# Optimization experiments

Hardware: AMD Instinct MI355X
Metric: run time of the kernel (lower is better)

Reference implementation:

```python
import jax, jax.numpy as jnp
import numpy as np

A = 20000        # distinct library arcs
T = 500000       # timing arcs in design
S = 8            # LUT slew-axis length
C = 8            # LUT load-axis length
G = 250000       # gates
TOTAL_U = 1000000  # gate x candidate-master entries
SCALE = 1.0e15
MAX_CAP = 1.0e-12
MAX_ITER = 3


def _axis_interval(ax, x):
    """ax: [M,K] monotone axes, x: [M]. Returns lower index i0 in [0,K-2] and frac a (may extrapolate)."""
    K = ax.shape[1]
    i0 = jnp.clip(jnp.sum(ax <= x[:, None], axis=1) - 1, 0, K - 2)
    ar = jnp.arange(ax.shape[0])
    x0 = ax[ar, i0]
    x1 = ax[ar, i0 + 1]
    a = (x - x0) / (x1 - x0)
    return i0, a


def _bilinear_gate(in_slew, load, dtab, stab, axs, axc):
    """Batched bilinear interpolation into per-arc 2D LUTs. All leading dims M."""
    M = in_slew.shape[0]
    ar = jnp.arange(M)
    i0, a = _axis_interval(axs, in_slew)
    j0, b = _axis_interval(axc, load)
    i1, j1 = i0 + 1, j0 + 1

    def _blerp(t):
        return ((1 - a) * (1 - b) * t[ar, i0, j0]
                + (1 - a) * b * t[ar, i0, j1]
                + a * (1 - b) * t[ar, i1, j0]
                + a * b * t[ar, i1, j1])

    return _blerp(dtab), _blerp(stab)


def _compute_ceff_batch(in_slew, c1, c2, rpi, dtab, stab, axs, axc, max_iter=MAX_ITER):
    ceff = jnp.maximum(c1 + c2, 1e-30)
    for _ in range(max_iter):
        d, _ = _bilinear_gate(in_slew, ceff, dtab, stab, axs, axc)
        tau = jnp.maximum(d, 1e-30)
        ratio = jnp.minimum(2.0 * tau / jnp.maximum(in_slew, 1e-30), 10.0)
        h = jnp.where(ratio > 0.01, (1.0 - jnp.exp(-ratio)) / ratio, 1.0 - ratio / 2.0)
        ceff = jnp.maximum(c1 + c2 * h, 1e-30)
    return ceff


def _segment_softmax(logits, gate_id, num_groups):
    """Numerically stable per-gate softmax via segment reductions."""
    gmax = jax.ops.segment_max(logits, gate_id, num_segments=num_groups)
    ex = jnp.exp(logits - gmax[gate_id])
    gsum = jax.ops.segment_sum(ex, gate_id, num_segments=num_groups)
    return ex / gsum[gate_id]


def _gate_grouped_forward(in_arr, in_slew, c1, c2, rpi, arc_idx_r, arc_idx_f,
                          unateness, delay_table, slew_table, load_index, slew_index):
    t = arc_idx_r.shape[0]
    arc_flat = jnp.stack([arc_idx_r, arc_idx_f], axis=1).reshape(-1)  # [2T]
    una = unateness[arc_flat]
    is_fall = jnp.arange(2 * t, dtype=una.dtype) % 2
    rf_idx = (una ^ is_fall).reshape(t, 2)  # rise/fall select per column
    in_slew_sel = jnp.take_along_axis(in_slew, rf_idx, axis=1).reshape(-1)
    in_arr_sel = jnp.take_along_axis(in_arr, rf_idx, axis=1).reshape(-1)

    dtab = delay_table[arc_flat]   # [2T,S,C] big gather (memory bound)
    stab = slew_table[arc_flat]
    axc = load_index[arc_flat]     # [2T,C]
    axs = slew_index[arc_flat]     # [2T,S]

    c1_f = jnp.repeat(c1, 2) / SCALE
    c2_f = jnp.repeat(c2, 2) / SCALE
    rpi_f = jnp.repeat(rpi, 2)
    load = _compute_ceff_batch(in_slew_sel, c1_f, c2_f, rpi_f, dtab, stab, axs, axc)
    load = jnp.minimum(load, MAX_CAP)

    arc_delay, arc_slew = _bilinear_gate(in_slew_sel, load, dtab, stab, axs, axc)
    arr_out = (in_arr_sel + arc_delay).reshape(t, 2)
    slew_out = arc_slew.reshape(t, 2)
    return jnp.concatenate([arr_out, slew_out], axis=1)  # [T,4]


def setup_inputs() -> dict:
    key = jax.random.key(0)
    ks = jax.random.split(key, 14)
    U_flat = jax.random.normal(ks[0], (TOTAL_U,), jnp.float32)
    gate_id = jnp.sort(jax.random.randint(ks[1], (TOTAL_U,), 0, G, dtype=jnp.int32))
    in_arr = jax.random.normal(ks[2], (T, 2), jnp.float32)
    in_slew = jax.random.uniform(ks[3], (T, 2), jnp.float32, 0.05, 3.0)
    c1 = jax.random.uniform(ks[4], (T,), jnp.float32, 0.0, 1.0)
    c2 = jax.random.uniform(ks[5], (T,), jnp.float32, 0.0, 1.0)
    rpi = jax.random.uniform(ks[6], (T,), jnp.float32, 0.1, 1.0)
    arc_idx_r = jax.random.randint(ks[7], (T,), 0, A, dtype=jnp.int32)
    arc_idx_f = jax.random.randint(ks[8], (T,), 0, A, dtype=jnp.int32)
    unateness = jax.random.randint(ks[9], (A,), 0, 2, dtype=jnp.int32)
    delay_table = jax.random.uniform(ks[10], (A, S, C), jnp.float32, 0.01, 1.0)
    slew_table = jax.random.uniform(ks[11], (A, S, C), jnp.float32, 0.01, 1.0)
    # strictly increasing LUT axes: slew axis ~[0.05, 4], load axis ~[5e-17, 3e-15]
    slew_index = jnp.cumsum(jax.random.uniform(ks[12], (A, S), jnp.float32, 0.05, 0.6), axis=1)
    load_index = jnp.cumsum(jax.random.uniform(ks[13], (A, C), jnp.float32, 0.05, 0.6), axis=1) * 1e-15
    return dict(U_flat=U_flat, gate_id=gate_id, in_arr=in_arr, in_slew=in_slew,
                c1=c1, c2=c2, rpi=rpi, arc_idx_r=arc_idx_r, arc_idx_f=arc_idx_f,
                unateness=unateness, delay_table=delay_table, slew_table=slew_table,
                slew_index=slew_index, load_index=load_index)


def reference(U_flat, gate_id, in_arr, in_slew, c1, c2, rpi, arc_idx_r, arc_idx_f,
              unateness, delay_table, slew_table, slew_index, load_index):
    weights = _segment_softmax(U_flat, gate_id, G)  # per-gate soft master selection
    out = _gate_grouped_forward(in_arr, in_slew, c1, c2, rpi, arc_idx_r, arc_idx_f,
                                unateness, delay_table, slew_table, load_index, slew_index)
    return out, weights
```

## Files before the change

### kernel.cpp

```cpp
#include <hip/hip_runtime.h>

#define T_N 500000
#define U_N 1000000
#define G_N 250000
#define A_N 20000

#define SBLK 256
#define HALO 96

#define TIMING_BLOCKS ((T_N + 255) / 256)
#define SOFTMAX_BLOCKS ((U_N + SBLK - 1) / SBLK)

__device__ __forceinline__ float sel8(const float (&r)[8], int j) {
    float v = r[0];
#pragma unroll
    for (int k = 1; k < 8; ++k) v = (j >= k) ? r[k] : v;
    return v;
}

__device__ __forceinline__ void load8(const float* __restrict__ p, float (&r)[8]) {
    const float4* q = (const float4*)p;
    float4 a = q[0], b = q[1];
    r[0]=a.x; r[1]=a.y; r[2]=a.z; r[3]=a.w;
    r[4]=b.x; r[5]=b.y; r[6]=b.z; r[7]=b.w;
}


__global__ void __launch_bounds__(256)
fused_kernel(
             const float2* __restrict__ in_arr,
             const float2* __restrict__ in_slew,
             const float* __restrict__ c1,
             const float* __restrict__ c2,
             const int* __restrict__ arc_r,
             const int* __restrict__ arc_f,
             const int* __restrict__ una,
             const float* __restrict__ dtab,
             const float* __restrict__ stab,
             const float* __restrict__ sidx,
             const float* __restrict__ lidx,
             float4* __restrict__ out,
             const float* __restrict__ U,
             const int* __restrict__ gid,
             float* __restrict__ wout)
{
    __shared__ float se[SBLK + 2 * HALO];
    __shared__ int   sg[SBLK + 2 * HALO];

    if (blockIdx.x >= TIMING_BLOCKS) {
        int sblk = blockIdx.x - TIMING_BLOCKS;
        int base = sblk * SBLK;
        int wstart = base - HALO;

        for (int k = threadIdx.x; k < SBLK + 2 * HALO; k += SBLK) {
            int idx = wstart + k;
            if (idx >= 0 && idx < U_N) {
                se[k] = expf(U[idx]);
                sg[k] = gid[idx];
            } else {
                se[k] = 0.0f;
                sg[k] = -1 - k;
            }
        }
        __syncthreads();

        int i = base + threadIdx.x;
        if (i >= U_N) return;

        int li = threadIdx.x + HALO;
        int g = sg[li];
        float mye = se[li];
        float s = mye;
        for (int j = li - 1; j >= 0 && sg[j] == g; --j) s += se[j];
        for (int j = li + 1; j < SBLK + 2 * HALO && sg[j] == g; ++j) s += se[j];

        wout[i] = mye / s;
        return;
    }

    int t = blockIdx.x * blockDim.x + threadIdx.x;
    if (t >= T_N) return;

    float2 ia = in_arr[t];
    float2 is = in_slew[t];
    float c1f = c1[t] / 1.0e15f;
    float c2f = c2[t] / 1.0e15f;
    int arcs0 = arc_r[t];
    int arcs1 = arc_f[t];

    float res_arr[2], res_slew[2];

#pragma unroll
    for (int col = 0; col < 2; ++col) {
        int arc = (col == 0) ? arcs0 : arcs1;
        int u   = una[arc];
        int rf  = u ^ col;
        float slew = rf ? is.y : is.x;
        float arr  = rf ? ia.y : ia.x;

        float s[8], cx[8];
        load8(sidx + (size_t)arc * 8, s);
        load8(lidx + (size_t)arc * 8, cx);

        int cnt = 0;
#pragma unroll
        for (int k = 0; k < 8; ++k) cnt += (s[k] <= slew) ? 1 : 0;
        int i0 = min(max(cnt - 1, 0), 6);
        float x0 = sel8(s, i0);
        float x1 = sel8(s, i0 + 1);
        float a = (slew - x0) / (x1 - x0);
        float om_a = 1.0f - a;

        float d0[8], d1[8];
        load8(dtab + (size_t)arc * 64 + (size_t)i0 * 8, d0);
        load8(dtab + (size_t)arc * 64 + (size_t)i0 * 8 + 8, d1);

        float slew_den = fmaxf(slew, 1e-30f);
        float ceff = fmaxf(c1f + c2f, 1e-30f);
#pragma unroll
        for (int it = 0; it < 3; ++it) {
            int jc = 0;
#pragma unroll
            for (int k = 0; k < 8; ++k) jc += (cx[k] <= ceff) ? 1 : 0;
            int j0 = min(max(jc - 1, 0), 6);
            float y0 = sel8(cx, j0);
            float y1 = sel8(cx, j0 + 1);
            float b = (ceff - y0) / (y1 - y0);
            float om_b = 1.0f - b;
            float v00 = sel8(d0, j0), v01 = sel8(d0, j0 + 1);
            float v10 = sel8(d1, j0), v11 = sel8(d1, j0 + 1);
            float d = om_a * om_b * v00 + om_a * b * v01
                    + a * om_b * v10 + a * b * v11;
            float tau = fmaxf(d, 1e-30f);
            float ratio = fminf(2.0f * tau / slew_den, 10.0f);
            float h = (ratio > 0.01f) ? (1.0f - expf(-ratio)) / ratio
                                      : 1.0f - 0.5f * ratio;
            ceff = fmaxf(c1f + c2f * h, 1e-30f);
        }
        float load = fminf(ceff, 1.0e-12f);

        int jc = 0;
#pragma unroll
        for (int k = 0; k < 8; ++k) jc += (cx[k] <= load) ? 1 : 0;
        int j0 = min(max(jc - 1, 0), 6);
        float y0 = sel8(cx, j0);
        float y1 = sel8(cx, j0 + 1);
        float b = (load - y0) / (y1 - y0);
        float om_b = 1.0f - b;

        float v00 = sel8(d0, j0), v01 = sel8(d0, j0 + 1);
        float v10 = sel8(d1, j0), v11 = sel8(d1, j0 + 1);
        float delay = om_a * om_b * v00 + om_a * b * v01
                    + a * om_b * v10 + a * b * v11;

        const float* srow = stab + (size_t)arc * 64 + (size_t)i0 * 8;
        float s00 = srow[j0],     s01 = srow[j0 + 1];
        float s10 = srow[8 + j0], s11 = srow[8 + j0 + 1];
        float sl = om_a * om_b * s00 + om_a * b * s01
                 + a * om_b * s10 + a * b * s11;

        res_arr[col]  = arr + delay;
        res_slew[col] = sl;
    }

    out[t] = make_float4(res_arr[0], res_arr[1], res_slew[0], res_slew[1]);
}

extern "C" void kernel_launch(void* const* d_in, const int* in_sizes, int n_in,
                              void* d_out, int out_size, void* d_ws, size_t ws_size,
                              hipStream_t stream) {
    const float*  U      = (const float*)d_in[0];
    const int*    gid    = (const int*)d_in[1];
    const float2* in_arr = (const float2*)d_in[2];
    const float2* in_slw = (const float2*)d_in[3];
    const float*  c1     = (const float*)d_in[4];
    const float*  c2     = (const float*)d_in[5];
    const int*    arc_r  = (const int*)d_in[7];
    const int*    arc_f  = (const int*)d_in[8];
    const int*    una    = (const int*)d_in[9];
    const float*  dtab   = (const float*)d_in[10];
    const float*  stab   = (const float*)d_in[11];
    const float*  sidx   = (const float*)d_in[12];
    const float*  lidx   = (const float*)d_in[13];

    float* out  = (float*)d_out;
    float* wout = out + (size_t)T_N * 4;

    fused_kernel<<<TIMING_BLOCKS + SOFTMAX_BLOCKS, 256, 0, stream>>>(
        in_arr, in_slw, c1, c2, arc_r, arc_f, una, dtab, stab, sidx, lidx,
        (float4*)out, U, gid, wout);
}
```

Baseline: 165.1 us.

## Split timing work to one thread per arc column and use nontemporal streaming loads

Each timing arc is now handled by two adjacent threads, one for the rise column and one for the fall column, instead of one thread doing both serially. The partner results are exchanged with a lane shuffle and the even lane writes the float4. Streaming inputs and outputs in both the timing and softmax paths now use nontemporal loads and stores to avoid cache pollution. This doubles thread count and latency-hiding parallelism for the gather-heavy LUT work, at the cost of loading per-arc inputs twice.

```diff
diff --git a/kernel.cpp b/kernel.cpp
--- a/kernel.cpp
+++ b/kernel.cpp
@@ -8,8 +8,12 @@
 #define SBLK 256
 #define HALO 96
 
-#define TIMING_BLOCKS ((T_N + 255) / 256)
+#define TIMING_THREADS (2 * T_N)
+#define TIMING_BLOCKS ((TIMING_THREADS + 255) / 256)
 #define SOFTMAX_BLOCKS ((U_N + SBLK - 1) / SBLK)
+
+typedef float vfloat2 __attribute__((ext_vector_type(2)));
+typedef float vfloat4 __attribute__((ext_vector_type(4)));
 
 __device__ __forceinline__ float sel8(const float (&r)[8], int j) {
     float v = r[0];
@@ -55,8 +59,8 @@
         for (int k = threadIdx.x; k < SBLK + 2 * HALO; k += SBLK) {
             int idx = wstart + k;
             if (idx >= 0 && idx < U_N) {
-                se[k] = expf(U[idx]);
-                sg[k] = gid[idx];
+                se[k] = expf(__builtin_nontemporal_load(U + idx));
+                sg[k] = __builtin_nontemporal_load(gid + idx);
             } else {
                 se[k] = 0.0f;
                 sg[k] = -1 - k;
@@ -74,96 +78,98 @@
         for (int j = li - 1; j >= 0 && sg[j] == g; --j) s += se[j];
         for (int j = li + 1; j < SBLK + 2 * HALO && sg[j] == g; ++j) s += se[j];
 
-        wout[i] = mye / s;
+        __builtin_nontemporal_store(mye / s, wout + i);
         return;
     }
 
-    int t = blockIdx.x * blockDim.x + threadIdx.x;
-    if (t >= T_N) return;
+    int v = blockIdx.x * blockDim.x + threadIdx.x;
+    if (v >= TIMING_THREADS) return;
+    int t   = v >> 1;
+    int col = v & 1;
 
-    float2 ia = in_arr[t];
-    float2 is = in_slew[t];
-    float c1f = c1[t] / 1.0e15f;
-    float c2f = c2[t] / 1.0e15f;
-    int arcs0 = arc_r[t];
-    int arcs1 = arc_f[t];
+    const int* __restrict__ arcp = col ? arc_f : arc_r;
+    int arc = __builtin_nontemporal_load(arcp + t);
 
-    float res_arr[2], res_slew[2];
+    vfloat2 is = __builtin_nontemporal_load((const vfloat2*)in_slew + t);
+    vfloat2 ia = __builtin_nontemporal_load((const vfloat2*)in_arr + t);
+    float c1f = __builtin_nontemporal_load(c1 + t) / 1.0e15f;
+    float c2f = __builtin_nontemporal_load(c2 + t) / 1.0e15f;
 
+    int u  = una[arc];
+    int rf = u ^ col;
+    float slew = rf ? is.y : is.x;
+    float arr  = rf ? ia.y : ia.x;
+
+    float s[8], cx[8];
+    load8(sidx + (size_t)arc * 8, s);
+    load8(lidx + (size_t)arc * 8, cx);
+
+    int cnt = 0;
 #pragma unroll
-    for (int col = 0; col < 2; ++col) {
-        int arc = (col == 0) ? arcs0 : arcs1;
-        int u   = una[arc];
-        int rf  = u ^ col;
-        float slew = rf ? is.y : is.x;
-        float arr  = rf ? ia.y : ia.x;
+    for (int k = 0; k < 8; ++k) cnt += (s[k] <= slew) ? 1 : 0;
+    int i0 = min(max(cnt - 1, 0), 6);
+    float x0 = sel8(s, i0);
+    float x1 = sel8(s, i0 + 1);
+    float a = (slew - x0) / (x1 - x0);
+    float om_a = 1.0f - a;
 
-        float s[8], cx[8];
-        load8(sidx + (size_t)arc * 8, s);
-        load8(lidx + (size_t)arc * 8, cx);
+    float d0[8], d1[8];
+    load8(dtab + (size_t)arc * 64 + (size_t)i0 * 8, d0);
+    load8(dtab + (size_t)arc * 64 + (size_t)i0 * 8 + 8, d1);
 
-        int cnt = 0;
+    float slew_den = fmaxf(slew, 1e-30f);
+    float ceff = fmaxf(c1f + c2f, 1e-30f);
 #pragma unroll
-        for (int k = 0; k < 8; ++k) cnt += (s[k] <= slew) ? 1 : 0;
-        int i0 = min(max(cnt - 1, 0), 6);
-        float x0 = sel8(s, i0);
-        float x1 = sel8(s, i0 + 1);
-        float a = (slew - x0) / (x1 - x0);
-        float om_a = 1.0f - a;
-
-        float d0[8], d1[8];
-        load8(dtab + (size_t)arc * 64 + (size_t)i0 * 8, d0);
-        load8(dtab + (size_t)arc * 64 + (size_t)i0 * 8 + 8, d1);
-
-        float slew_den = fmaxf(slew, 1e-30f);
-        float ceff = fmaxf(c1f + c2f, 1e-30f);
-#pragma unroll
-        for (int it = 0; it < 3; ++it) {
-            int jc = 0;
-#pragma unroll
-            for (int k = 0; k < 8; ++k) jc += (cx[k] <= ceff) ? 1 : 0;
-            int j0 = min(max(jc - 1, 0), 6);
-            float y0 = sel8(cx, j0);
-            float y1 = sel8(cx, j0 + 1);
-            float b = (ceff - y0) / (y1 - y0);
-            float om_b = 1.0f - b;
-            float v00 = sel8(d0, j0), v01 = sel8(d0, j0 + 1);
-            float v10 = sel8(d1, j0), v11 = sel8(d1, j0 + 1);
-            float d = om_a * om_b * v00 + om_a * b * v01
-                    + a * om_b * v10 + a * b * v11;
-            float tau = fmaxf(d, 1e-30f);
-            float ratio = fminf(2.0f * tau / slew_den, 10.0f);
-            float h = (ratio > 0.01f) ? (1.0f - expf(-ratio)) / ratio
-                                      : 1.0f - 0.5f * ratio;
-            ceff = fmaxf(c1f + c2f * h, 1e-30f);
-        }
-        float load = fminf(ceff, 1.0e-12f);
-
+    for (int it = 0; it < 3; ++it) {
         int jc = 0;
 #pragma unroll
-        for (int k = 0; k < 8; ++k) jc += (cx[k] <= load) ? 1 : 0;
+        for (int k = 0; k < 8; ++k) jc += (cx[k] <= ceff) ? 1 : 0;
         int j0 = min(max(jc - 1, 0), 6);
         float y0 = sel8(cx, j0);
         float y1 = sel8(cx, j0 + 1);
-        float b = (load - y0) / (y1 - y0);
+        float b = (ceff - y0) / (y1 - y0);
         float om_b = 1.0f - b;
-
         float v00 = sel8(d0, j0), v01 = sel8(d0, j0 + 1);
         float v10 = sel8(d1, j0), v11 = sel8(d1, j0 + 1);
-        float delay = om_a * om_b * v00 + om_a * b * v01
-                    + a * om_b * v10 + a * b * v11;
+        float d = om_a * om_b * v00 + om_a * b * v01
+                + a * om_b * v10 + a * b * v11;
+        float tau = fmaxf(d, 1e-30f);
+        float ratio = fminf(2.0f * tau / slew_den, 10.0f);
+        float h = (ratio > 0.01f) ? (1.0f - expf(-ratio)) / ratio
+                                  : 1.0f - 0.5f * ratio;
+        ceff = fmaxf(c1f + c2f * h, 1e-30f);
+    }
+    float load = fminf(ceff, 1.0e-12f);
 
-        const float* srow = stab + (size_t)arc * 64 + (size_t)i0 * 8;
-        float s00 = srow[j0],     s01 = srow[j0 + 1];
-        float s10 = srow[8 + j0], s11 = srow[8 + j0 + 1];
-        float sl = om_a * om_b * s00 + om_a * b * s01
-                 + a * om_b * s10 + a * b * s11;
+    int jc = 0;
+#pragma unroll
+    for (int k = 0; k < 8; ++k) jc += (cx[k] <= load) ? 1 : 0;
+    int j0 = min(max(jc - 1, 0), 6);
+    float y0 = sel8(cx, j0);
+    float y1 = sel8(cx, j0 + 1);
+    float b = (load - y0) / (y1 - y0);
+    float om_b = 1.0f - b;
 
-        res_arr[col]  = arr + delay;
-        res_slew[col] = sl;
+    float v00 = sel8(d0, j0), v01 = sel8(d0, j0 + 1);
+    float v10 = sel8(d1, j0), v11 = sel8(d1, j0 + 1);
+    float delay = om_a * om_b * v00 + om_a * b * v01
+                + a * om_b * v10 + a * b * v11;
+
+    const float* srow = stab + (size_t)arc * 64 + (size_t)i0 * 8;
+    float s00 = srow[j0],     s01 = srow[j0 + 1];
+    float s10 = srow[8 + j0], s11 = srow[8 + j0 + 1];
+    float sl = om_a * om_b * s00 + om_a * b * s01
+             + a * om_b * s10 + a * b * s11;
+
+    float res_a = arr + delay;
+    float res_s = sl;
+
+    float oa = __shfl_xor(res_a, 1);
+    float os = __shfl_xor(res_s, 1);
+    if (col == 0) {
+        vfloat4 o = {res_a, oa, res_s, os};
+        __builtin_nontemporal_store(o, (vfloat4*)out + t);
     }
-
-    out[t] = make_float4(res_arr[0], res_arr[1], res_slew[0], res_slew[1]);
 }
 
 extern "C" void kernel_launch(void* const* d_in, const int* in_sizes, int n_in,
```

Result: slower. 172.8 us (+4.7%).
